# Performance work log

Hardware: AMD Instinct MI355X
Metric: run time of the kernel (lower is better)

The kernel has to match this reference:

```python
import jax, jax.numpy as jnp
import numpy as np

VOXEL_SIZE = jnp.array([0.075, 0.075], dtype=jnp.float32)
PC_RANGE = jnp.array([-54.0, -54.0], dtype=jnp.float32)
FUSION_STRIDE = 8.0
SRC_STRIDES = (4.0, 8.0)
RADII = (2.4, 4.8)
NSAMPLE = 16
NKEY = 500


def _mlp(x, w1, g1, b1, w2, b2):
    # Linear(no bias) + BatchNorm(eval, running mean=0/var=1 -> affine) + ReLU, then Linear
    h = jax.nn.relu((x @ w1) * g1 + b1)
    return h @ w2 + b2


def _world(coords, stride):
    # voxel coord -> world xy center
    return (coords.astype(jnp.float32) + 0.5) * stride * VOXEL_SIZE + PC_RANGE


def _gather_rows(x, idx):
    # x: (B, N, ...), idx: (B, ...) -> per-batch row gather
    return jax.vmap(lambda f, i: f[i])(x, idx)


def _knn(key_world, src_world, src_feat, radius):
    # key_world (B,Nk,2), src_world (B,Ns,2), src_feat (B,Ns,C)
    d2 = jnp.sum((key_world[:, :, None, :] - src_world[:, None, :, :]) ** 2, axis=-1)  # (B,Nk,Ns)
    d2 = jnp.where(d2 <= radius * radius, d2, jnp.inf)
    negd, idx = jax.lax.top_k(-d2, NSAMPLE)  # nearest NSAMPLE within radius, (B,Nk,K)
    valid = jnp.isfinite(negd).astype(src_feat.dtype)  # empty==0 mask
    feats = _gather_rows(src_feat, idx)  # (B,Nk,K,C)
    return feats * valid[..., None]


def setup_inputs() -> dict:
    key = jax.random.key(0)
    ks = jax.random.split(key, 24)
    s = 0.05
    return {
        'fusion_feat': jax.random.normal(ks[0], (2, 20000, 128), jnp.float32),
        'src_feat_a': jax.random.normal(ks[1], (2, 30000, 128), jnp.float32),
        'src_feat_b': jax.random.normal(ks[2], (2, 30000, 128), jnp.float32),
        'heat_w1': jax.random.normal(ks[3], (128, 128), jnp.float32) * s,
        'heat_g1': jnp.ones((128,), jnp.float32),
        'heat_b1': jnp.zeros((128,), jnp.float32),
        'heat_w2': jax.random.normal(ks[4], (128, 10), jnp.float32) * s,
        'heat_b2': jnp.zeros((10,), jnp.float32),
        'knn_w': jax.random.normal(ks[5], (2, 16), jnp.float32) * s,
        'knn_b': jnp.zeros((2,), jnp.float32),
        'kw_w1': jax.random.normal(ks[6], (128, 64), jnp.float32) * s,
        'kw_g1': jnp.ones((64,), jnp.float32),
        'kw_b1': jnp.zeros((64,), jnp.float32),
        'kw_w2': jax.random.normal(ks[7], (64, 3), jnp.float32) * s,
        'kw_b2': jnp.zeros((3,), jnp.float32),
        'fuse_w1': jax.random.normal(ks[8], (256, 256), jnp.float32) * s,
        'fuse_g1': jnp.ones((256,), jnp.float32),
        'fuse_b1': jnp.zeros((256,), jnp.float32),
        'fuse_w2': jax.random.normal(ks[9], (256, 128), jnp.float32) * s,
        'fuse_b2': jnp.zeros((128,), jnp.float32),
        'fusion_coords': jax.random.randint(ks[10], (2, 20000, 2), 0, 180, jnp.int32),
        'src_coords_a': jax.random.randint(ks[11], (2, 30000, 2), 0, 360, jnp.int32),
        'src_coords_b': jax.random.randint(ks[12], (2, 30000, 2), 0, 180, jnp.int32),
    }


def reference(fusion_feat, src_feat_a, src_feat_b, heat_w1, heat_g1, heat_b1,
              heat_w2, heat_b2, knn_w, knn_b, kw_w1, kw_g1, kw_b1, kw_w2, kw_b2,
              fuse_w1, fuse_g1, fuse_b1, fuse_w2, fuse_b2,
              fusion_coords, src_coords_a, src_coords_b):
    B = fusion_feat.shape[0]
    # heatmap head over all fusion voxels
    scores10 = _mlp(fusion_feat, heat_w1, heat_g1, heat_b1, heat_w2, heat_b2)  # (B,Nf,10)
    heat_scores = jnp.max(scores10, axis=-1)
    cls = jnp.argmax(scores10, axis=-1)
    # per-sample top-k key voxel selection
    _, tki = jax.lax.top_k(jax.nn.sigmoid(heat_scores), NKEY)  # (B,Nk)
    key_feat = _gather_rows(fusion_feat, tki)      # (B,Nk,128)
    key_coords = _gather_rows(fusion_coords, tki)  # (B,Nk,2)
    key_class = _gather_rows(cls, tki)             # (B,Nk)
    key_world = _world(key_coords, FUSION_STRIDE)  # (B,Nk,2)

    srcs = ((src_feat_a, src_coords_a), (src_feat_b, src_coords_b))
    mlp_feats = []
    for s, (sf, sc) in enumerate(srcs):
        sw = _world(sc, SRC_STRIDES[s])
        kf = _knn(key_world, sw, sf, RADII[s])  # (B,Nk,K,C), zeroed where empty
        # Linear over the K neighbor axis (knn_feat_mlp: NSAMPLE -> 1)
        mf = jnp.einsum('bnkc,k->bnc', kf, knn_w[s]) + knn_b[s]
        mlp_feats.append(mf)

    w = jax.nn.softmax(_mlp(key_feat, kw_w1, kw_g1, kw_b1, kw_w2, kw_b2), axis=-1)  # (B,Nk,3)
    # faithful to original: key_voxel_feat is re-scaled cumulatively inside the loop
    kvf = key_feat
    fuse_sum = jnp.zeros_like(key_feat)
    for i in range(len(srcs)):
        kvf = w[..., i:i + 1] * kvf
        fuse_sum = fuse_sum + kvf * mlp_feats[i]
    fused = jnp.concatenate([fuse_sum, kvf], axis=-1)  # (B,Nk,256)
    out = _mlp(fused, fuse_w1, fuse_g1, fuse_b1, fuse_w2, fuse_b2)  # (B,Nk,128)

    bs_col = jnp.broadcast_to(jnp.arange(B, dtype=key_coords.dtype)[:, None, None], (B, NKEY, 1))
    key_voxel_indices = jnp.concatenate([bs_col, key_coords], axis=-1).reshape(B * NKEY, 3)
    return (out.reshape(B * NKEY, -1), key_voxel_indices,
            heat_scores.reshape(-1), scores10.reshape(-1, scores10.shape[-1]), key_class)
```

## Files before the change

kernel.cpp:

```cpp
#include <hip/hip_runtime.h>
#include <math.h>

#define BB 2
#define NF 20000
#define NS 30000
#define CH 128
#define NK 500
#define KNN 16
#define KPB 4

#define HA 2.4024f
#define HB 4.8048f
#define NCA 45
#define NCB 23
#define CELLS_A 2025
#define CELLS_B 529

#define OUT0_OFF 0
#define OUT1_OFF 128000
#define OUT2_OFF 131000
#define OUT3_OFF 171000
#define OUT4_OFF 571000

#define WS_CLS   0
#define WS_TKI   160000
#define WS_KW    164000
#define WS_MF    172000
#define WS_KEYS  WS_MF
#define WS_GSTART 1196000
#define WS_PTS    1236880
#define WS_PIDX   2196880

#define STB(s,b)  ((s) ? (4052 + (b) * 530) : ((b) * 2026))

__device__ __forceinline__ void fma4(float4& acc, float sc, const float4& wv) {
    acc.x += sc * wv.x; acc.y += sc * wv.y;
    acc.z += sc * wv.z; acc.w += sc * wv.w;
}

__device__ __forceinline__ unsigned ordf(float s) {
    unsigned u = __float_as_uint(s);
    return (u & 0x80000000u) ? ~u : (u | 0x80000000u);
}

__device__ __forceinline__ void world_cell_sb(
    const int2* sc, int s, int i, float& sx, float& sy, int& cell)
{
    int2 c = sc[i];
    float stride = s ? 8.0f : 4.0f;
    sx = __fadd_rn(__fmul_rn(__fmul_rn(__fadd_rn((float)c.x, 0.5f), stride), 0.075f), -54.0f);
    sy = __fadd_rn(__fmul_rn(__fmul_rn(__fadd_rn((float)c.y, 0.5f), stride), 0.075f), -54.0f);
    float inv_h = s ? (1.0f / HB) : (1.0f / HA);
    int nc = s ? NCB : NCA;
    int cx = (int)floorf((sx + 54.0f) * inv_h);
    int cy = (int)floorf((sy + 54.0f) * inv_h);
    cx = min(max(cx, 0), nc - 1);
    cy = min(max(cy, 0), nc - 1);
    cell = cy * nc + cx;
}

__global__ __launch_bounds__(256) void heat_kernel(
    const float* __restrict__ x,
    const float* __restrict__ w1,
    const float* __restrict__ g1, const float* __restrict__ b1,
    const float* __restrict__ w2,
    const float* __restrict__ b2,
    float* __restrict__ out_heat,
    float* __restrict__ out_s10,
    int* __restrict__ cls,
    unsigned long long* __restrict__ keys)
{
    __shared__ float As[64 * 72];
    __shared__ float Ws[64 * 132];
    __shared__ float W2s[1280];
    const int tid = threadIdx.x;
    const int m0 = blockIdx.x * 64;
    const int tx = tid & 15;
    const int ty = tid >> 4;

    for (int v = tid; v < 1280; v += 256) W2s[v] = w2[v];

    float acc[4][8];
#pragma unroll
    for (int i = 0; i < 4; ++i)
#pragma unroll
        for (int j = 0; j < 8; ++j) acc[i][j] = 0.f;

    const float4* xv = (const float4*)x;
    const float4* w1v = (const float4*)w1;

    for (int kc = 0; kc < 128; kc += 64) {
#pragma unroll
        for (int i = 0; i < 4; ++i) {
            int v = tid + i * 256;
            int row = v >> 4, c4 = v & 15;
            float4 val = xv[(size_t)(m0 + row) * 32 + (kc >> 2) + c4];
            *(float4*)&As[row * 72 + c4 * 4] = val;
        }
#pragma unroll
        for (int i = 0; i < 8; ++i) {
            int v = tid + i * 256;
            int k = v >> 5, c4 = v & 31;
            float4 val = w1v[(size_t)(kc + k) * 32 + c4];
            *(float4*)&Ws[k * 132 + c4 * 4] = val;
        }
        __syncthreads();

        const float* a0p = &As[(ty * 4 + 0) * 72];
        const float* a1p = &As[(ty * 4 + 1) * 72];
        const float* a2p = &As[(ty * 4 + 2) * 72];
        const float* a3p = &As[(ty * 4 + 3) * 72];
#pragma unroll 4
        for (int k = 0; k < 64; ++k) {
            float4 bA = *(const float4*)&Ws[k * 132 + tx * 8];
            float4 bB = *(const float4*)&Ws[k * 132 + tx * 8 + 4];
            float a0 = a0p[k], a1 = a1p[k], a2 = a2p[k], a3 = a3p[k];
            acc[0][0] += a0 * bA.x; acc[0][1] += a0 * bA.y; acc[0][2] += a0 * bA.z; acc[0][3] += a0 * bA.w;
            acc[0][4] += a0 * bB.x; acc[0][5] += a0 * bB.y; acc[0][6] += a0 * bB.z; acc[0][7] += a0 * bB.w;
            acc[1][0] += a1 * bA.x; acc[1][1] += a1 * bA.y; acc[1][2] += a1 * bA.z; acc[1][3] += a1 * bA.w;
            acc[1][4] += a1 * bB.x; acc[1][5] += a1 * bB.y; acc[1][6] += a1 * bB.z; acc[1][7] += a1 * bB.w;
            acc[2][0] += a2 * bA.x; acc[2][1] += a2 * bA.y; acc[2][2] += a2 * bA.z; acc[2][3] += a2 * bA.w;
            acc[2][4] += a2 * bB.x; acc[2][5] += a2 * bB.y; acc[2][6] += a2 * bB.z; acc[2][7] += a2 * bB.w;
            acc[3][0] += a3 * bA.x; acc[3][1] += a3 * bA.y; acc[3][2] += a3 * bA.z; acc[3][3] += a3 * bA.w;
            acc[3][4] += a3 * bB.x; acc[3][5] += a3 * bB.y; acc[3][6] += a3 * bB.z; acc[3][7] += a3 * bB.w;
        }
        __syncthreads();
    }

    float4 g1a = ((const float4*)g1)[tx * 2], g1b = ((const float4*)g1)[tx * 2 + 1];
    float4 b1a = ((const float4*)b1)[tx * 2], b1b = ((const float4*)b1)[tx * 2 + 1];
    float* Hs = Ws;
#pragma unroll
    for (int i = 0; i < 4; ++i) {
        int row = ty * 4 + i;
        float4 hA, hB;
        hA.x = fmaxf(acc[i][0] * g1a.x + b1a.x, 0.f);
        hA.y = fmaxf(acc[i][1] * g1a.y + b1a.y, 0.f);
        hA.z = fmaxf(acc[i][2] * g1a.z + b1a.z, 0.f);
        hA.w = fmaxf(acc[i][3] * g1a.w + b1a.w, 0.f);
        hB.x = fmaxf(acc[i][4] * g1b.x + b1b.x, 0.f);
        hB.y = fmaxf(acc[i][5] * g1b.y + b1b.y, 0.f);
        hB.z = fmaxf(acc[i][6] * g1b.z + b1b.z, 0.f);
        hB.w = fmaxf(acc[i][7] * g1b.w + b1b.w, 0.f);
        *(float4*)&Hs[row * 132 + tx * 8] = hA;
        *(float4*)&Hs[row * 132 + tx * 8 + 4] = hB;
    }
    __syncthreads();

    const int r = tid >> 2;
    const int p = tid & 3;
    float a2[10];
#pragma unroll
    for (int c = 0; c < 10; ++c) a2[c] = 0.f;
    for (int kk = 0; kk < 32; ++kk) {
        int k = kk * 4 + p;
        float hv = Hs[r * 132 + k];
#pragma unroll
        for (int c = 0; c < 10; ++c) a2[c] += hv * W2s[k * 10 + c];
    }
#pragma unroll
    for (int c = 0; c < 10; ++c) {
        a2[c] += __shfl_xor(a2[c], 1);
        a2[c] += __shfl_xor(a2[c], 2);
    }
    if (p == 0) {
        int m = m0 + r;
        float best = -INFINITY;
        int bi = 0;
#pragma unroll
        for (int c = 0; c < 10; ++c) {
            float s = a2[c] + b2[c];
            out_s10[(size_t)m * 10 + c] = s;
            if (s > best) { best = s; bi = c; }
        }
        out_heat[m] = best;
        cls[m] = bi;
        int b = m / NF;
        unsigned i = (unsigned)(m - b * NF);
        float sig = 1.0f / (1.0f + expf(-best));
        keys[m] = ((unsigned long long)ordf(sig) << 32) | (unsigned)(~i);
    }
}

#define H1BINS 16384

__global__ __launch_bounds__(1024) void mid_kernel(
    const unsigned long long* __restrict__ keys,
    const int* __restrict__ cls,
    const int* __restrict__ fcoords,
    float* __restrict__ out1,
    float* __restrict__ out4,
    int* __restrict__ tki,
    float* __restrict__ keyworld,
    const int* __restrict__ sca, const int* __restrict__ scb,
    int* __restrict__ gstart,
    float2* __restrict__ pts, int* __restrict__ pidx)
{
    __shared__ unsigned h[H1BINS];
    __shared__ unsigned sA[1024], sB[1024];
    __shared__ unsigned long long list[1024];
    __shared__ unsigned chunk_s, aboveC_s, T1_s, aboveT1_s, cand_s, thr_s, cnt_s;
    __shared__ int ghist[2048];
    const int tid = threadIdx.x;
    const int blk = blockIdx.x;

    if (blk >= 2) {
        const int g = blk - 2;
        const int s = g >> 1, b = g & 1;
        const int n = s ? CELLS_B : CELLS_A;
        const int stb = STB(s, b);
        const int2* sc = ((const int2*)(s ? scb : sca)) + (size_t)b * NS;
        const size_t pbase = ((size_t)s * BB + b) * NS;
        int* gt0 = (int*)sA;
        int* gt1 = (int*)sB;

        for (int i = tid; i < 2048; i += 1024) ghist[i] = 0;
        __syncthreads();
        for (int i = tid; i < NS; i += 1024) {
            float sx, sy; int cell;
            world_cell_sb(sc, s, i, sx, sy, cell);
            atomicAdd(&ghist[cell], 1);
        }
        __syncthreads();
        int i0 = tid * 2, i1 = tid * 2 + 1;
        int c0 = (i0 < n) ? ghist[i0] : 0;
        int c1 = (i1 < n) ? ghist[i1] : 0;
        gt0[tid] = c0 + c1;
        __syncthreads();
        int* srcp = gt0; int* dstp = gt1;
        for (int off = 1; off < 1024; off <<= 1) {
            int v = srcp[tid];
            if (tid >= off) v += srcp[tid - off];
            dstp[tid] = v;
            __syncthreads();
            int* t = srcp; srcp = dstp; dstp = t;
        }
        int excl = (tid == 0) ? 0 : srcp[tid - 1];
        if (i0 < n) { gstart[stb + i0] = excl; ghist[i0] = excl; }
        if (i1 < n) { gstart[stb + i1] = excl + c0; ghist[i1] = excl + c0; }
        if (tid == 0) gstart[stb + n] = NS;
        __syncthreads();
        for (int i = tid; i < NS; i += 1024) {
            float sx, sy; int cell;
            world_cell_sb(sc, s, i, sx, sy, cell);
            int pos = atomicAdd(&ghist[cell], 1);
            pts[pbase + pos] = make_float2(sx, sy);
            pidx[pbase + pos] = i;
        }
        return;
    }

    const int b = blk;
    const unsigned long long* kb = keys + (size_t)b * NF;
    const unsigned K = NK;

    for (int i = tid; i < H1BINS; i += 1024) h[i] = 0u;
    __syncthreads();
#pragma unroll 4
    for (int i = tid; i < NF; i += 1024)
        atomicAdd(&h[(unsigned)(kb[i] >> 50)], 1u);
    __syncthreads();
    unsigned ck = 0;
    {
        int base = tid * 16;
#pragma unroll
        for (int j = 0; j < 16; ++j) ck += h[base + j];
        sA[tid] = ck;
    }
    __syncthreads();
    unsigned* srcp = sA; unsigned* dstp = sB;
    for (int off = 1; off < 1024; off <<= 1) {
        unsigned v = srcp[tid];
        if (tid + off < 1024) v += srcp[tid + off];
        dstp[tid] = v;
        __syncthreads();
        unsigned* t = srcp; srcp = dstp; dstp = t;
    }
    {
        unsigned suf = srcp[tid];
        unsigned above = suf - ck;
        if (above < K && K <= suf) { chunk_s = (unsigned)tid; aboveC_s = above; }
    }
    __syncthreads();
    if (tid == 0) {
        int bin = (int)chunk_s * 16 + 15;
        unsigned acc = aboveC_s;
        for (;; --bin) { if (acc + h[bin] >= K) break; acc += h[bin]; }
        T1_s = (unsigned)bin;
        aboveT1_s = acc;
        cand_s = acc + h[bin];
        cnt_s = 0u;
    }
    __syncthreads();
    const unsigned T1 = T1_s;

    if (cand_s <= 1024u) {
#pragma unroll 4
        for (int i = tid; i < NF; i += 1024) {
            unsigned long long key = kb[i];
            if ((unsigned)(key >> 50) >= T1) {
                unsigned pos = atomicAdd(&cnt_s, 1u);
                if (pos < 1024u) list[pos] = key;
            }
        }
    } else {
        const unsigned K2 = K - aboveT1_s;
        h[tid] = 0u;
        __syncthreads();
#pragma unroll 4
        for (int i = tid; i < NF; i += 1024) {
            unsigned long long key = kb[i];
            if ((unsigned)(key >> 50) == T1)
                atomicAdd(&h[(unsigned)(key >> 40) & 1023u], 1u);
        }
        __syncthreads();
        unsigned hb = h[tid];
        sA[tid] = hb;
        __syncthreads();
        unsigned* s2 = sA; unsigned* d2 = sB;
        for (int off = 1; off < 1024; off <<= 1) {
            unsigned v = s2[tid];
            if (tid + off < 1024) v += s2[tid + off];
            d2[tid] = v;
            __syncthreads();
            unsigned* t = s2; s2 = d2; d2 = t;
        }
        {
            unsigned suf = s2[tid];
            unsigned above = suf - hb;
            if (above < K2 && K2 <= suf) thr_s = (T1 << 10) | (unsigned)tid;
        }
        __syncthreads();
        const unsigned thr24 = thr_s;
#pragma unroll 4
        for (int i = tid; i < NF; i += 1024) {
            unsigned long long key = kb[i];
            if ((unsigned)(key >> 40) >= thr24) {
                unsigned pos = atomicAdd(&cnt_s, 1u);
                if (pos < 1024u) list[pos] = key;
            }
        }
    }
    __syncthreads();
    const int cc = (int)(cnt_s > 1024u ? 1024u : cnt_s);

    if (tid < cc) {
        unsigned long long mykey = list[tid];
        unsigned r = 0;
#pragma unroll 8
        for (int j = 0; j < cc; ++j) r += (list[j] > mykey) ? 1u : 0u;
        if (r < (unsigned)NK) {
            int idx = (int)(~(unsigned)(mykey & 0xFFFFFFFFull));
            tki[b * NK + (int)r] = idx;
            int c0 = fcoords[((size_t)b * NF + idx) * 2 + 0];
            int c1 = fcoords[((size_t)b * NF + idx) * 2 + 1];
            size_t o = (size_t)(b * NK + (int)r);
            out1[o * 3 + 0] = (float)b;
            out1[o * 3 + 1] = (float)c0;
            out1[o * 3 + 2] = (float)c1;
            float wx = __fadd_rn(__fmul_rn(__fmul_rn(__fadd_rn((float)c0, 0.5f), 8.0f), 0.075f), -54.0f);
            float wy = __fadd_rn(__fmul_rn(__fmul_rn(__fadd_rn((float)c1, 0.5f), 8.0f), 0.075f), -54.0f);
            keyworld[o * 2 + 0] = wx;
            keyworld[o * 2 + 1] = wy;
            out4[o] = (float)cls[(size_t)b * NF + idx];
        }
    }
}

__global__ __launch_bounds__(256) void knn_kernel(
    const float* __restrict__ sfa, const float* __restrict__ sfb,
    const int* __restrict__ gstart,
    const float2* __restrict__ pts, const int* __restrict__ pidx,
    const float* __restrict__ knn_w,
    const float* __restrict__ knn_b,
    const float* __restrict__ keyworld,
    float* __restrict__ mf)
{
    __shared__ unsigned long long list[1024];
    __shared__ float psum[128];
    __shared__ unsigned cnt_s;
    const int tid = threadIdx.x;
    const int blk = blockIdx.x;
    const int s = blk / (BB * NK);
    const int rest = blk % (BB * NK);
    const int b = rest / NK;
    const int r = rest % NK;
    const float* sfeat = s ? sfb : sfa;
    const float r2 = s ? (float)(4.8 * 4.8) : (float)(2.4 * 2.4);
    const float inv_h = s ? (1.0f / HB) : (1.0f / HA);
    const int nc = s ? NCB : NCA;
    const int stb = STB(s, b);
    const size_t pbase = ((size_t)s * BB + b) * NS;

    if (tid == 0) cnt_s = 0u;
    __syncthreads();
    const float kx = keyworld[((size_t)b * NK + r) * 2 + 0];
    const float ky = keyworld[((size_t)b * NK + r) * 2 + 1];
    int cx = (int)floorf((kx + 54.0f) * inv_h);
    int cy = (int)floorf((ky + 54.0f) * inv_h);
    cx = min(max(cx, 0), nc - 1);
    cy = min(max(cy, 0), nc - 1);
    const int c0 = max(cx - 1, 0), c1 = min(cx + 1, nc - 1);
    const int cy0 = max(cy - 1, 0), cy1 = min(cy + 1, nc - 1);

    for (int cyy = cy0; cyy <= cy1; ++cyy) {
        int lo = gstart[stb + cyy * nc + c0];
        int hi = gstart[stb + cyy * nc + c1 + 1];
        for (int p = lo + tid; p < hi; p += 256) {
            float2 w = pts[pbase + p];
            float dx = __fsub_rn(kx, w.x);
            float dy = __fsub_rn(ky, w.y);
            float d2 = __fadd_rn(__fmul_rn(dx, dx), __fmul_rn(dy, dy));
            if (d2 <= r2) {
                unsigned pos = atomicAdd(&cnt_s, 1u);
                if (pos < 1024u)
                    list[pos] = ((unsigned long long)__float_as_uint(d2) << 32)
                              | (unsigned)pidx[pbase + p];
            }
        }
    }
    __syncthreads();
    int cc = (int)cnt_s;
    if (cc > 1024) cc = 1024;
    int n2 = 16;
    while (n2 < cc) n2 <<= 1;
    for (int i = tid; i < n2; i += 256)
        if (i >= cc) list[i] = ~0ull;
    __syncthreads();
    for (int kk = 2; kk <= n2; kk <<= 1) {
        for (int j = kk >> 1; j > 0; j >>= 1) {
            for (int i = tid; i < n2; i += 256) {
                int ixj = i ^ j;
                if (ixj > i) {
                    unsigned long long a = list[i], bv = list[ixj];
                    bool up = ((i & kk) == 0);
                    bool sw = up ? (a > bv) : (a < bv);
                    if (sw) { list[i] = bv; list[ixj] = a; }
                }
            }
            __syncthreads();
        }
    }
    {
        int K = cc < KNN ? cc : KNN;
        int col = tid & 127, half = tid >> 7;
        float acc = 0.f;
        int k0 = half * 8, k1 = min(K, half * 8 + 8);
        for (int k = k0; k < k1; ++k) {
            unsigned i = (unsigned)(list[k] & 0xFFFFFFFFull);
            acc += knn_w[s * 16 + k] * sfeat[((size_t)b * NS + i) * CH + col];
        }
        if (half) psum[col] = acc;
        __syncthreads();
        if (!half)
            mf[(((size_t)s * BB + b) * NK + r) * CH + col] = knn_b[s] + acc + psum[col];
    }
}

__global__ __launch_bounds__(1024) void fuse_kernel(
    const float* __restrict__ ffeat,
    const int* __restrict__ tki,
    const float* __restrict__ kw_w1, const float* __restrict__ kw_g1,
    const float* __restrict__ kw_b1, const float* __restrict__ kw_w2,
    const float* __restrict__ kw_b2,
    const float* __restrict__ fuse_w1, const float* __restrict__ fuse_g1,
    const float* __restrict__ fuse_b1, const float* __restrict__ fuse_w2,
    const float* __restrict__ fuse_b2,
    const float* __restrict__ mf,
    float* __restrict__ out0)
{
    __shared__ float pL[16384];
    __shared__ float xsT[512];
    __shared__ float mfs[1024];
    __shared__ float fusedvT[1024];
    __shared__ float h2sT[1024];
    __shared__ float prm[964];
    __shared__ float hsX[256];
    __shared__ float p2[96];
    __shared__ float l3[12];
    __shared__ float wsm[8];
    __shared__ int idxs[KPB], bs[KPB], rs[KPB];
    const int tid = threadIdx.x;
    const int f0 = blockIdx.x * KPB;

    if (tid < 964) {
        float v;
        if (tid < 64)       v = kw_g1[tid];
        else if (tid < 128) v = kw_b1[tid - 64];
        else if (tid < 320) v = kw_w2[tid - 128];
        else if (tid < 323) v = kw_b2[tid - 320];
        else if (tid < 324) v = 0.f;
        else if (tid < 580) v = fuse_g1[tid - 324];
        else if (tid < 836) v = fuse_b1[tid - 580];
        else                v = fuse_b2[tid - 836];
        prm[tid] = v;
    }
    if (tid < KPB) {
        int flat = f0 + tid;
        int b = flat / NK;
        bs[tid] = b;
        rs[tid] = flat - b * NK;
        idxs[tid] = tki[flat];
    }
    __syncthreads();

    if (tid < 128) {
        int key = tid >> 5, c4 = tid & 31;
        float4 v = ((const float4*)(ffeat + ((size_t)bs[key] * NF + idxs[key]) * CH))[c4];
        xsT[(c4 * 4 + 0) * 4 + key] = v.x;
        xsT[(c4 * 4 + 1) * 4 + key] = v.y;
        xsT[(c4 * 4 + 2) * 4 + key] = v.z;
        xsT[(c4 * 4 + 3) * 4 + key] = v.w;
    }
    if (tid < 256) {
        int ss = tid >> 7, key = (tid >> 5) & 3, c4 = tid & 31;
        float4 v = ((const float4*)(mf + (((size_t)ss * BB + bs[key]) * NK + rs[key]) * CH))[c4];
        *(float4*)&mfs[ss * 512 + key * 128 + c4 * 4] = v;
    }
    __syncthreads();

    if (tid < 256) {
        const int og = tid & 15, kseg = tid >> 4;
        float4 wr[8];
#pragma unroll
        for (int m = 0; m < 8; ++m)
            wr[m] = ((const float4*)kw_w1)[(kseg * 8 + m) * 16 + og];
        float4 a0 = {0, 0, 0, 0}, a1 = {0, 0, 0, 0}, a2 = {0, 0, 0, 0}, a3 = {0, 0, 0, 0};
#pragma unroll
        for (int m = 0; m < 8; ++m) {
            float4 f4 = *(const float4*)&xsT[(kseg * 8 + m) * 4];
            fma4(a0, f4.x, wr[m]);
            fma4(a1, f4.y, wr[m]);
            fma4(a2, f4.z, wr[m]);
            fma4(a3, f4.w, wr[m]);
        }
        *(float4*)&pL[(kseg * 4 + 0) * 64 + og * 4] = a0;
        *(float4*)&pL[(kseg * 4 + 1) * 64 + og * 4] = a1;
        *(float4*)&pL[(kseg * 4 + 2) * 64 + og * 4] = a2;
        *(float4*)&pL[(kseg * 4 + 3) * 64 + og * 4] = a3;
    }
    __syncthreads();
    if (tid < 256) {
        int out = tid >> 2, key = tid & 3;
        float s = 0.f;
#pragma unroll
        for (int ks = 0; ks < 16; ++ks) s += pL[(ks * 4 + key) * 64 + out];
        float t = s * prm[out] + prm[64 + out];
        hsX[key * 64 + out] = t > 0.f ? t : 0.f;
    }
    __syncthreads();
    if (tid < 96) {
        int key = tid / 24, rr = tid % 24, out = rr >> 3, seg = rr & 7;
        float acc = 0.f;
#pragma unroll
        for (int m = 0; m < 8; ++m) {
            int k = seg * 8 + m;
            acc += hsX[key * 64 + k] * prm[128 + k * 3 + out];
        }
        p2[(key * 3 + out) * 8 + seg] = acc;
    }
    __syncthreads();
    if (tid < 12) {
        int key = tid / 3, out = tid % 3;
        float s = 0.f;
#pragma unroll
        for (int j = 0; j < 8; ++j) s += p2[(key * 3 + out) * 8 + j];
        l3[key * 3 + out] = s + prm[320 + out];
    }
    __syncthreads();
    if (tid < KPB) {
        float l0 = l3[tid * 3], l1 = l3[tid * 3 + 1], l2 = l3[tid * 3 + 2];
        float m = fmaxf(l0, fmaxf(l1, l2));
        float e0 = expf(l0 - m), e1 = expf(l1 - m), e2 = expf(l2 - m);
        float sum = e0 + e1 + e2;
        wsm[tid * 2 + 0] = e0 / sum;
        wsm[tid * 2 + 1] = e1 / sum;
    }
    __syncthreads();

    {
        int c = tid >> 2, key = tid & 3;
        float w0 = wsm[key * 2], w1_ = wsm[key * 2 + 1];
        float val;
        if (c < 128) {
            float xv_ = xsT[c * 4 + key];
            float m0 = mfs[key * 128 + c];
            float m1 = mfs[512 + key * 128 + c];
            float kv = w0 * xv_;
            float kv2 = w1_ * kv;
            val = kv * m0 + kv2 * m1;
        } else {
            float xv_ = xsT[(c - 128) * 4 + key];
            val = w1_ * (w0 * xv_);
        }
        fusedvT[tid] = val;
    }
    __syncthreads();

    {
        const int og = tid & 63, kseg = tid >> 6;
        const float4* w1v = (const float4*)fuse_w1;
        float4 wr[16];
#pragma unroll
        for (int m = 0; m < 16; ++m)
            wr[m] = w1v[(kseg * 16 + m) * 64 + og];
        float4 a0 = {0, 0, 0, 0}, a1 = {0, 0, 0, 0}, a2 = {0, 0, 0, 0}, a3 = {0, 0, 0, 0};
#pragma unroll
        for (int m = 0; m < 16; ++m) {
            float4 f4 = *(const float4*)&fusedvT[(kseg * 16 + m) * 4];
            fma4(a0, f4.x, wr[m]);
            fma4(a1, f4.y, wr[m]);
            fma4(a2, f4.z, wr[m]);
            fma4(a3, f4.w, wr[m]);
        }
        *(float4*)&pL[(kseg * 4 + 0) * 256 + og * 4] = a0;
        *(float4*)&pL[(kseg * 4 + 1) * 256 + og * 4] = a1;
        *(float4*)&pL[(kseg * 4 + 2) * 256 + og * 4] = a2;
        *(float4*)&pL[(kseg * 4 + 3) * 256 + og * 4] = a3;
    }
    __syncthreads();
    {
        int out = tid >> 2, key = tid & 3;
        float s = 0.f;
#pragma unroll
        for (int ks = 0; ks < 16; ++ks) s += pL[(ks * 4 + key) * 256 + out];
        float t = s * prm[324 + out] + prm[580 + out];
        h2sT[out * 4 + key] = t > 0.f ? t : 0.f;
    }
    __syncthreads();

    {
        const int og2 = tid & 31, kseg2 = tid >> 5;
        const float4* w2v = (const float4*)fuse_w2;
        float4 wr[8];
#pragma unroll
        for (int m = 0; m < 8; ++m)
            wr[m] = w2v[(kseg2 * 8 + m) * 32 + og2];
        float4 a0 = {0, 0, 0, 0}, a1 = {0, 0, 0, 0}, a2 = {0, 0, 0, 0}, a3 = {0, 0, 0, 0};
#pragma unroll
        for (int m = 0; m < 8; ++m) {
            float4 f4 = *(const float4*)&h2sT[(kseg2 * 8 + m) * 4];
            fma4(a0, f4.x, wr[m]);
            fma4(a1, f4.y, wr[m]);
            fma4(a2, f4.z, wr[m]);
            fma4(a3, f4.w, wr[m]);
        }
        *(float4*)&pL[(kseg2 * 4 + 0) * 128 + og2 * 4] = a0;
        *(float4*)&pL[(kseg2 * 4 + 1) * 128 + og2 * 4] = a1;
        *(float4*)&pL[(kseg2 * 4 + 2) * 128 + og2 * 4] = a2;
        *(float4*)&pL[(kseg2 * 4 + 3) * 128 + og2 * 4] = a3;
    }
    __syncthreads();
    if (tid < 512) {
        int out = tid >> 2, key = tid & 3;
        float s = prm[836 + out];
#pragma unroll
        for (int ks = 0; ks < 32; ++ks) s += pL[(ks * 4 + key) * 128 + out];
        out0[((size_t)bs[key] * NK + rs[key]) * CH + out] = s;
    }
}

extern "C" void kernel_launch(void* const* d_in, const int* in_sizes, int n_in,
                              void* d_out, int out_size, void* d_ws, size_t ws_size,
                              hipStream_t stream)
{
    const float* fusion_feat = (const float*)d_in[0];
    const float* src_feat_a  = (const float*)d_in[1];
    const float* src_feat_b  = (const float*)d_in[2];
    const float* heat_w1 = (const float*)d_in[3];
    const float* heat_g1 = (const float*)d_in[4];
    const float* heat_b1 = (const float*)d_in[5];
    const float* heat_w2 = (const float*)d_in[6];
    const float* heat_b2 = (const float*)d_in[7];
    const float* knn_w   = (const float*)d_in[8];
    const float* knn_b   = (const float*)d_in[9];
    const float* kw_w1   = (const float*)d_in[10];
    const float* kw_g1   = (const float*)d_in[11];
    const float* kw_b1   = (const float*)d_in[12];
    const float* kw_w2   = (const float*)d_in[13];
    const float* kw_b2   = (const float*)d_in[14];
    const float* fuse_w1 = (const float*)d_in[15];
    const float* fuse_g1 = (const float*)d_in[16];
    const float* fuse_b1 = (const float*)d_in[17];
    const float* fuse_w2 = (const float*)d_in[18];
    const float* fuse_b2 = (const float*)d_in[19];
    const int* fusion_coords = (const int*)d_in[20];
    const int* src_coords_a  = (const int*)d_in[21];
    const int* src_coords_b  = (const int*)d_in[22];

    float* out = (float*)d_out;
    char* ws = (char*)d_ws;
    int* cls = (int*)(ws + WS_CLS);
    int* tki = (int*)(ws + WS_TKI);
    float* keyworld = (float*)(ws + WS_KW);
    float* mf = (float*)(ws + WS_MF);
    unsigned long long* keys = (unsigned long long*)(ws + WS_KEYS);
    int* gstart = (int*)(ws + WS_GSTART);
    float2* pts = (float2*)(ws + WS_PTS);
    int* pidx = (int*)(ws + WS_PIDX);

    heat_kernel<<<(BB * NF) / 64, 256, 0, stream>>>(
        fusion_feat, heat_w1, heat_g1, heat_b1, heat_w2, heat_b2,
        out + OUT2_OFF, out + OUT3_OFF, cls, keys);

    mid_kernel<<<6, 1024, 0, stream>>>(
        keys, cls, fusion_coords,
        out + OUT1_OFF, out + OUT4_OFF, tki, keyworld,
        src_coords_a, src_coords_b, gstart, pts, pidx);

    knn_kernel<<<2 * BB * NK, 256, 0, stream>>>(
        src_feat_a, src_feat_b, gstart, pts, pidx,
        knn_w, knn_b, keyworld, mf);

    fuse_kernel<<<(BB * NK) / KPB, 1024, 0, stream>>>(
        fusion_feat, tki, kw_w1, kw_g1, kw_b1, kw_w2, kw_b2,
        fuse_w1, fuse_g1, fuse_b1, fuse_w2, fuse_b2, mf, out + OUT0_OFF);
}
```

Before: 245.4 us.

## Move source-point grid bucketing into heat kernel's extra blocks

The counting-sort bucketing of source points into spatial cells moves from the mid_kernel (1024-thread blocks) into four extra 256-thread blocks at the front of the heat_kernel grid. The bucketing then runs alongside the heat GEMM, and mid_kernel only does the top-k selection, which shortens the serial top-k stage. In exchange, the bucketing blocks have fewer threads, use an 8-per-thread scan, and reuse the GEMM's shared arrays as scratch, so they may take longer per block and could extend the heat kernel's tail.

```diff
diff --git a/kernel.cpp b/kernel.cpp
--- a/kernel.cpp
+++ b/kernel.cpp
@@ -68,13 +68,75 @@
     float* __restrict__ out_heat,
     float* __restrict__ out_s10,
     int* __restrict__ cls,
-    unsigned long long* __restrict__ keys)
+    unsigned long long* __restrict__ keys,
+    const int* __restrict__ sca, const int* __restrict__ scb,
+    int* __restrict__ gstart,
+    float2* __restrict__ pts, int* __restrict__ pidx)
 {
     __shared__ float As[64 * 72];
     __shared__ float Ws[64 * 132];
     __shared__ float W2s[1280];
     const int tid = threadIdx.x;
-    const int m0 = blockIdx.x * 64;
+
+    if (blockIdx.x < 4) {
+        const int g = blockIdx.x;
+        const int s = g >> 1, b = g & 1;
+        const int n = s ? CELLS_B : CELLS_A;
+        const int stb = STB(s, b);
+        const int2* sc = ((const int2*)(s ? scb : sca)) + (size_t)b * NS;
+        const size_t pbase = ((size_t)s * BB + b) * NS;
+        int* ghist = (int*)As;
+        int* sc0 = (int*)Ws;
+        int* sc1 = ((int*)Ws) + 256;
+
+        for (int i = tid; i < 2048; i += 256) ghist[i] = 0;
+        __syncthreads();
+        for (int i = tid; i < NS; i += 256) {
+            float sx, sy; int cell;
+            world_cell_sb(sc, s, i, sx, sy, cell);
+            atomicAdd(&ghist[cell], 1);
+        }
+        __syncthreads();
+        int cnt[8]; int tot = 0;
+#pragma unroll
+        for (int j = 0; j < 8; ++j) {
+            int idx = tid * 8 + j;
+            cnt[j] = (idx < n) ? ghist[idx] : 0;
+            tot += cnt[j];
+        }
+        sc0[tid] = tot;
+        __syncthreads();
+        int* srcp = sc0; int* dstp = sc1;
+        for (int off = 1; off < 256; off <<= 1) {
+            int v = srcp[tid];
+            if (tid >= off) v += srcp[tid - off];
+            dstp[tid] = v;
+            __syncthreads();
+            int* t = srcp; srcp = dstp; dstp = t;
+        }
+        int run = (tid == 0) ? 0 : srcp[tid - 1];
+#pragma unroll
+        for (int j = 0; j < 8; ++j) {
+            int idx = tid * 8 + j;
+            if (idx < n) {
+                gstart[stb + idx] = run;
+                ghist[idx] = run;
+                run += cnt[j];
+            }
+        }
+        if (tid == 0) gstart[stb + n] = NS;
+        __syncthreads();
+        for (int i = tid; i < NS; i += 256) {
+            float sx, sy; int cell;
+            world_cell_sb(sc, s, i, sx, sy, cell);
+            int pos = atomicAdd(&ghist[cell], 1);
+            pts[pbase + pos] = make_float2(sx, sy);
+            pidx[pbase + pos] = i;
+        }
+        return;
+    }
+
+    const int m0 = (blockIdx.x - 4) * 64;
     const int tx = tid & 15;
     const int ty = tid >> 4;
 
@@ -191,66 +253,15 @@
     float* __restrict__ out1,
     float* __restrict__ out4,
     int* __restrict__ tki,
-    float* __restrict__ keyworld,
-    const int* __restrict__ sca, const int* __restrict__ scb,
-    int* __restrict__ gstart,
-    float2* __restrict__ pts, int* __restrict__ pidx)
+    float* __restrict__ keyworld)
 {
     __shared__ unsigned h[H1BINS];
     __shared__ unsigned sA[1024], sB[1024];
     __shared__ unsigned long long list[1024];
     __shared__ unsigned chunk_s, aboveC_s, T1_s, aboveT1_s, cand_s, thr_s, cnt_s;
-    __shared__ int ghist[2048];
     const int tid = threadIdx.x;
-    const int blk = blockIdx.x;
-
-    if (blk >= 2) {
-        const int g = blk - 2;
-        const int s = g >> 1, b = g & 1;
-        const int n = s ? CELLS_B : CELLS_A;
-        const int stb = STB(s, b);
-        const int2* sc = ((const int2*)(s ? scb : sca)) + (size_t)b * NS;
-        const size_t pbase = ((size_t)s * BB + b) * NS;
-        int* gt0 = (int*)sA;
-        int* gt1 = (int*)sB;
-
-        for (int i = tid; i < 2048; i += 1024) ghist[i] = 0;
-        __syncthreads();
-        for (int i = tid; i < NS; i += 1024) {
-            float sx, sy; int cell;
-            world_cell_sb(sc, s, i, sx, sy, cell);
-            atomicAdd(&ghist[cell], 1);
-        }
-        __syncthreads();
-        int i0 = tid * 2, i1 = tid * 2 + 1;
-        int c0 = (i0 < n) ? ghist[i0] : 0;
-        int c1 = (i1 < n) ? ghist[i1] : 0;
-        gt0[tid] = c0 + c1;
-        __syncthreads();
-        int* srcp = gt0; int* dstp = gt1;
-        for (int off = 1; off < 1024; off <<= 1) {
-            int v = srcp[tid];
-            if (tid >= off) v += srcp[tid - off];
-            dstp[tid] = v;
-            __syncthreads();
-            int* t = srcp; srcp = dstp; dstp = t;
-        }
-        int excl = (tid == 0) ? 0 : srcp[tid - 1];
-        if (i0 < n) { gstart[stb + i0] = excl; ghist[i0] = excl; }
-        if (i1 < n) { gstart[stb + i1] = excl + c0; ghist[i1] = excl + c0; }
-        if (tid == 0) gstart[stb + n] = NS;
-        __syncthreads();
-        for (int i = tid; i < NS; i += 1024) {
-            float sx, sy; int cell;
-            world_cell_sb(sc, s, i, sx, sy, cell);
-            int pos = atomicAdd(&ghist[cell], 1);
-            pts[pbase + pos] = make_float2(sx, sy);
-            pidx[pbase + pos] = i;
-        }
-        return;
-    }
-
-    const int b = blk;
+
+    const int b = blockIdx.x;
     const unsigned long long* kb = keys + (size_t)b * NF;
     const unsigned K = NK;
 
@@ -699,14 +710,14 @@
     float2* pts = (float2*)(ws + WS_PTS);
     int* pidx = (int*)(ws + WS_PIDX);
 
-    heat_kernel<<<(BB * NF) / 64, 256, 0, stream>>>(
+    heat_kernel<<<(BB * NF) / 64 + 4, 256, 0, stream>>>(
         fusion_feat, heat_w1, heat_g1, heat_b1, heat_w2, heat_b2,
-        out + OUT2_OFF, out + OUT3_OFF, cls, keys);
-
-    mid_kernel<<<6, 1024, 0, stream>>>(
+        out + OUT2_OFF, out + OUT3_OFF, cls, keys,
+        src_coords_a, src_coords_b, gstart, pts, pidx);
+
+    mid_kernel<<<2, 1024, 0, stream>>>(
         keys, cls, fusion_coords,
-        out + OUT1_OFF, out + OUT4_OFF, tki, keyworld,
-        src_coords_a, src_coords_b, gstart, pts, pidx);
+        out + OUT1_OFF, out + OUT4_OFF, tki, keyworld);
 
     knn_kernel<<<2 * BB * NK, 256, 0, stream>>>(
         src_feat_a, src_feat_b, gstart, pts, pidx,
```

New measurement: 280.5 us. 14.3% more time.

## Split grid counting-sort across slices with histograms computed in heat kernel

Applied to the files above, without the earlier changes.

The spatial-hash counting sort of source points previously ran in four 1024-thread blocks, each doing histogram, scan and scatter over 30000 points. Now per-slice histograms are computed by 32 extra blocks inside the heat kernel. Then 32 mid-kernel blocks each combine the slice histograms, scan them, and scatter their own slice using prefix offsets. This spreads a serial-ish critical path across more CUs and overlaps histogramming with the heat GEMM, at the cost of a global histogram buffer and redundant scans per slice.

```diff
diff --git a/kernel.cpp b/kernel.cpp
--- a/kernel.cpp
+++ b/kernel.cpp
@@ -16,6 +16,10 @@
 #define CELLS_A 2025
 #define CELLS_B 529
 
+#define GB 8
+#define SLICE 3750
+#define SLICE4 1875
+
 #define OUT0_OFF 0
 #define OUT1_OFF 128000
 #define OUT2_OFF 131000
@@ -27,6 +31,7 @@
 #define WS_KW    164000
 #define WS_MF    172000
 #define WS_KEYS  WS_MF
+#define WS_BH    492000
 #define WS_GSTART 1196000
 #define WS_PTS    1236880
 #define WS_PIDX   2196880
@@ -43,20 +48,16 @@
     return (u & 0x80000000u) ? ~u : (u | 0x80000000u);
 }
 
-__device__ __forceinline__ void world_cell_sb(
-    const int2* sc, int s, int i, float& sx, float& sy, int& cell)
+__device__ __forceinline__ int cell_of(int cxi, int cyi, float stride, float inv_h,
+                                       int nc, float& sx, float& sy)
 {
-    int2 c = sc[i];
-    float stride = s ? 8.0f : 4.0f;
-    sx = __fadd_rn(__fmul_rn(__fmul_rn(__fadd_rn((float)c.x, 0.5f), stride), 0.075f), -54.0f);
-    sy = __fadd_rn(__fmul_rn(__fmul_rn(__fadd_rn((float)c.y, 0.5f), stride), 0.075f), -54.0f);
-    float inv_h = s ? (1.0f / HB) : (1.0f / HA);
-    int nc = s ? NCB : NCA;
+    sx = __fadd_rn(__fmul_rn(__fmul_rn(__fadd_rn((float)cxi, 0.5f), stride), 0.075f), -54.0f);
+    sy = __fadd_rn(__fmul_rn(__fmul_rn(__fadd_rn((float)cyi, 0.5f), stride), 0.075f), -54.0f);
     int cx = (int)floorf((sx + 54.0f) * inv_h);
     int cy = (int)floorf((sy + 54.0f) * inv_h);
     cx = min(max(cx, 0), nc - 1);
     cy = min(max(cy, 0), nc - 1);
-    cell = cy * nc + cx;
+    return cy * nc + cx;
 }
 
 __global__ __launch_bounds__(256) void heat_kernel(
@@ -68,13 +69,44 @@
     float* __restrict__ out_heat,
     float* __restrict__ out_s10,
     int* __restrict__ cls,
-    unsigned long long* __restrict__ keys)
+    unsigned long long* __restrict__ keys,
+    const int* __restrict__ sca, const int* __restrict__ scb,
+    int* __restrict__ bh)
 {
     __shared__ float As[64 * 72];
     __shared__ float Ws[64 * 132];
     __shared__ float W2s[1280];
     const int tid = threadIdx.x;
-    const int m0 = blockIdx.x * 64;
+
+    if (blockIdx.x < 4 * GB) {
+        const int gflat = blockIdx.x;
+        const int sb = gflat >> 3;
+        const int gg = gflat & (GB - 1);
+        const int s = sb >> 1, b = sb & 1;
+        const float stride = s ? 8.0f : 4.0f;
+        const float inv_h = s ? (1.0f / HB) : (1.0f / HA);
+        const int nc = s ? NCB : NCA;
+        const int2* sc = ((const int2*)(s ? scb : sca)) + (size_t)b * NS;
+        const int4* scv = (const int4*)sc;
+        int* hist = (int*)As;
+
+        for (int i = tid; i < 2048; i += 256) hist[i] = 0;
+        __syncthreads();
+        for (int p = gg * SLICE4 + tid; p < (gg + 1) * SLICE4; p += 256) {
+            int4 v = scv[p];
+            float sx, sy;
+            int cell0 = cell_of(v.x, v.y, stride, inv_h, nc, sx, sy);
+            int cell1 = cell_of(v.z, v.w, stride, inv_h, nc, sx, sy);
+            atomicAdd(&hist[cell0], 1);
+            atomicAdd(&hist[cell1], 1);
+        }
+        __syncthreads();
+        int* bhp = bh + (gflat << 11);
+        for (int i = tid; i < 2048; i += 256) bhp[i] = hist[i];
+        return;
+    }
+
+    const int m0 = (blockIdx.x - 4 * GB) * 64;
     const int tx = tid & 15;
     const int ty = tid >> 4;
 
@@ -193,6 +225,7 @@
     int* __restrict__ tki,
     float* __restrict__ keyworld,
     const int* __restrict__ sca, const int* __restrict__ scb,
+    const int* __restrict__ bh,
     int* __restrict__ gstart,
     float2* __restrict__ pts, int* __restrict__ pidx)
 {
@@ -200,34 +233,46 @@
     __shared__ unsigned sA[1024], sB[1024];
     __shared__ unsigned long long list[1024];
     __shared__ unsigned chunk_s, aboveC_s, T1_s, aboveT1_s, cand_s, thr_s, cnt_s;
-    __shared__ int ghist[2048];
     const int tid = threadIdx.x;
     const int blk = blockIdx.x;
 
     if (blk >= 2) {
-        const int g = blk - 2;
-        const int s = g >> 1, b = g & 1;
+        const int idx = blk - 2;
+        const int sb = idx >> 3;
+        const int j = idx & (GB - 1);
+        const int s = sb >> 1, b = sb & 1;
         const int n = s ? CELLS_B : CELLS_A;
+        const int nc = s ? NCB : NCA;
+        const float stride = s ? 8.0f : 4.0f;
+        const float inv_h = s ? (1.0f / HB) : (1.0f / HA);
         const int stb = STB(s, b);
         const int2* sc = ((const int2*)(s ? scb : sca)) + (size_t)b * NS;
+        const int4* scv = (const int4*)sc;
         const size_t pbase = ((size_t)s * BB + b) * NS;
-        int* gt0 = (int*)sA;
-        int* gt1 = (int*)sB;
-
-        for (int i = tid; i < 2048; i += 1024) ghist[i] = 0;
-        __syncthreads();
-        for (int i = tid; i < NS; i += 1024) {
-            float sx, sy; int cell;
-            world_cell_sb(sc, s, i, sx, sy, cell);
-            atomicAdd(&ghist[cell], 1);
-        }
-        __syncthreads();
-        int i0 = tid * 2, i1 = tid * 2 + 1;
-        int c0 = (i0 < n) ? ghist[i0] : 0;
-        int c1 = (i1 < n) ? ghist[i1] : 0;
-        gt0[tid] = c0 + c1;
-        __syncthreads();
-        int* srcp = gt0; int* dstp = gt1;
+        const int* bhsb = bh + (sb << 14);
+        int* tot = (int*)h;
+        int* cur = ((int*)h) + 2048;
+        int* scn0 = (int*)sA;
+        int* scn1 = (int*)sB;
+
+        for (int c = tid; c < 2048; c += 1024) {
+            int t = 0, pr = 0;
+#pragma unroll
+            for (int g = 0; g < GB; ++g) {
+                int v = bhsb[(g << 11) + c];
+                t += v;
+                if (g < j) pr += v;
+            }
+            tot[c] = t;
+            cur[c] = pr;
+        }
+        __syncthreads();
+        const int i0 = tid * 2, i1 = tid * 2 + 1;
+        int c0 = (i0 < n) ? tot[i0] : 0;
+        int c1 = (i1 < n) ? tot[i1] : 0;
+        scn0[tid] = c0 + c1;
+        __syncthreads();
+        int* srcp = scn0; int* dstp = scn1;
         for (int off = 1; off < 1024; off <<= 1) {
             int v = srcp[tid];
             if (tid >= off) v += srcp[tid - off];
@@ -235,17 +280,28 @@
             __syncthreads();
             int* t = srcp; srcp = dstp; dstp = t;
         }
-        int excl = (tid == 0) ? 0 : srcp[tid - 1];
-        if (i0 < n) { gstart[stb + i0] = excl; ghist[i0] = excl; }
-        if (i1 < n) { gstart[stb + i1] = excl + c0; ghist[i1] = excl + c0; }
-        if (tid == 0) gstart[stb + n] = NS;
-        __syncthreads();
-        for (int i = tid; i < NS; i += 1024) {
-            float sx, sy; int cell;
-            world_cell_sb(sc, s, i, sx, sy, cell);
-            int pos = atomicAdd(&ghist[cell], 1);
-            pts[pbase + pos] = make_float2(sx, sy);
-            pidx[pbase + pos] = i;
+        const int excl = (tid == 0) ? 0 : srcp[tid - 1];
+        if (i0 < n) {
+            if (j == 0) gstart[stb + i0] = excl;
+            cur[i0] += excl;
+        }
+        if (i1 < n) {
+            if (j == 0) gstart[stb + i1] = excl + c0;
+            cur[i1] += excl + c0;
+        }
+        if (j == 0 && tid == 0) gstart[stb + n] = NS;
+        __syncthreads();
+        for (int p = j * SLICE4 + tid; p < (j + 1) * SLICE4; p += 1024) {
+            int4 v = scv[p];
+            float sx0, sy0, sx1, sy1;
+            int cell0 = cell_of(v.x, v.y, stride, inv_h, nc, sx0, sy0);
+            int cell1 = cell_of(v.z, v.w, stride, inv_h, nc, sx1, sy1);
+            int pos0 = atomicAdd(&cur[cell0], 1);
+            int pos1 = atomicAdd(&cur[cell1], 1);
+            pts[pbase + pos0] = make_float2(sx0, sy0);
+            pidx[pbase + pos0] = p * 2;
+            pts[pbase + pos1] = make_float2(sx1, sy1);
+            pidx[pbase + pos1] = p * 2 + 1;
         }
         return;
     }
@@ -695,18 +751,20 @@
     float* keyworld = (float*)(ws + WS_KW);
     float* mf = (float*)(ws + WS_MF);
     unsigned long long* keys = (unsigned long long*)(ws + WS_KEYS);
+    int* bh = (int*)(ws + WS_BH);
     int* gstart = (int*)(ws + WS_GSTART);
     float2* pts = (float2*)(ws + WS_PTS);
     int* pidx = (int*)(ws + WS_PIDX);
 
-    heat_kernel<<<(BB * NF) / 64, 256, 0, stream>>>(
+    heat_kernel<<<(BB * NF) / 64 + 4 * GB, 256, 0, stream>>>(
         fusion_feat, heat_w1, heat_g1, heat_b1, heat_w2, heat_b2,
-        out + OUT2_OFF, out + OUT3_OFF, cls, keys);
-
-    mid_kernel<<<6, 1024, 0, stream>>>(
+        out + OUT2_OFF, out + OUT3_OFF, cls, keys,
+        src_coords_a, src_coords_b, bh);
+
+    mid_kernel<<<2 + 4 * GB, 1024, 0, stream>>>(
         keys, cls, fusion_coords,
         out + OUT1_OFF, out + OUT4_OFF, tki, keyworld,
-        src_coords_a, src_coords_b, gstart, pts, pidx);
+        src_coords_a, src_coords_b, bh, gstart, pts, pidx);
 
     knn_kernel<<<2 * BB * NK, 256, 0, stream>>>(
         src_feat_a, src_feat_b, gstart, pts, pidx,
```

New measurement: 232.1 us. -5.4%, faster.
